# Optimization experiments

Hardware: AMD Instinct MI355X
Metric: run time of the kernel (lower is better)

## Reference

```python
import jax, jax.numpy as jnp
import numpy as np

# ---- static config ----
SCALES = [1, 2, 3, 4, 6, 9, 13, 19, 27, 40, 60, 88, 128]
L = sum(SCALES)            # 400
FIRST_L = SCALES[0]        # 1
C = 1024                   # emb_dim (C == D)
DEPTH = 8
H = 16
DH = C // H
CVAE = 64
V = 4096
ND = 256                   # node_embed_size
MLP = 4 * C
B = 32
EPS = 1e-6

_LVL = np.concatenate([np.full(pn, i, dtype=np.int32) for i, pn in enumerate(SCALES)])  # [L]
_BIAS = np.where(_LVL[:, None] >= _LVL[None, :], 0.0, -np.inf).astype(np.float32)        # [L,L]


def _ln(x):
    # LayerNorm without affine params (VAR's ln_wo_grad), eps=1e-6
    m = jnp.mean(x, axis=-1, keepdims=True)
    v = jnp.mean(jnp.square(x - m), axis=-1, keepdims=True)
    return (x - m) * jax.lax.rsqrt(v + EPS)


def setup_inputs() -> dict:
    key = jax.random.key(0)
    ks = iter(jax.random.split(key, 40))
    def p(shape, s=0.02):
        return jax.random.normal(next(ks), shape, dtype=jnp.float32) * s
    inp = {
        "x_BLCv_wo_first_l": jax.random.normal(next(ks), (B, L - FIRST_L, CVAE), jnp.float32),
        "poc_context": jax.random.normal(next(ks), (B, L, CVAE), jnp.float32),
        "poc_cond": jax.random.normal(next(ks), (B, ND), jnp.float32),
        # embedders / positional
        "word_w": p((CVAE, C)), "word_b": p((C,)),
        "poc_w": p((ND, C)), "poc_b": p((C,)),
        "pos_start": p((1, FIRST_L, C)),
        "pos_1LC": p((1, L, C)),
        "lvl_tab": p((len(SCALES), C)),
        # shared AdaLN (SiLU -> Linear(D, 6C))
        "ada_w": p((C, 6 * C)), "ada_b": p((6 * C,)),
        # per-block params, stacked over depth
        "ada_gss": p((DEPTH, 1, 1, 6, C)),
        "q_w": p((DEPTH, C, C)), "q_b": p((DEPTH, C)),
        "kv_w": p((DEPTH, C, 2 * C)), "kv_b": p((DEPTH, 2 * C)),
        "proj_w": p((DEPTH, C, C)), "proj_b": p((DEPTH, C)),
        "fc1_w": p((DEPTH, C, MLP)), "fc1_b": p((DEPTH, MLP)),
        "fc2_w": p((DEPTH, MLP, C)), "fc2_b": p((DEPTH, C)),
        # AdaLNBeforeHead (SiLU -> Linear(D, 2C)) + head
        "head_ada_w": p((C, 2 * C)), "head_ada_b": p((2 * C,)),
        "head_w": p((C, V)), "head_b": p((V,)),
    }
    return inp


def reference(x_BLCv_wo_first_l, poc_context, poc_cond,
              word_w, word_b, poc_w, poc_b, pos_start, pos_1LC, lvl_tab,
              ada_w, ada_b, ada_gss, q_w, q_b, kv_w, kv_b, proj_w, proj_b,
              fc1_w, fc1_b, fc2_w, fc2_b, head_ada_w, head_ada_b, head_w, head_b):
    lvl_idx = jnp.asarray(_LVL)
    bias = jnp.asarray(_BIAS)                      # [L,L] block scale-causal
    scale = 1.0 / np.sqrt(DH)

    cond = poc_cond @ poc_w + poc_b                # [B,C] (cond_BD == sos source)
    sos = cond[:, None, :] + pos_start             # [B,first_l,C]
    x = jnp.concatenate([sos, x_BLCv_wo_first_l @ word_w + word_b], axis=1)  # [B,L,C]
    lvl = lvl_tab[lvl_idx] + pos_1LC[0]            # [L,C]
    x = x + lvl
    poc = (poc_context @ word_w + word_b) + lvl    # [B,L,C]

    gss = jax.nn.silu(cond) @ ada_w + ada_b        # [B,6C]
    gss = gss.reshape(B, 1, 6, C)

    def block(x, params):
        ag, qw, qb, kvw, kvb, pw, pb, f1w, f1b, f2w, f2b = params
        mod = ag + gss                             # [B,1,6,C]
        g1, g2, s1, s2, sh1, sh2 = [mod[:, :, i] for i in range(6)]  # each [B,1,C]
        # cross-attention (q from modulated x, kv from poc context), scale-causal bias
        xn = _ln(x) * (1.0 + s1) + sh1
        q = (xn @ qw + qb).reshape(B, L, H, DH)
        kv = (poc @ kvw + kvb).reshape(B, L, 2, H, DH)
        k, v = kv[:, :, 0], kv[:, :, 1]
        att = jnp.einsum('bqhd,bkhd->bhqk', q, k) * scale + bias
        att = jax.nn.softmax(att, axis=-1)
        o = jnp.einsum('bhqk,bkhd->bqhd', att, v).reshape(B, L, C)
        x = x + g1 * (o @ pw + pb)
        # FFN with AdaLN modulation
        xn2 = _ln(x) * (1.0 + s2) + sh2
        hdn = jax.nn.gelu(xn2 @ f1w + f1b, approximate=False)
        x = x + g2 * (hdn @ f2w + f2b)
        return x, None

    x, _ = jax.lax.scan(block, x, (ada_gss, q_w, q_b, kv_w, kv_b, proj_w, proj_b,
                                   fc1_w, fc1_b, fc2_w, fc2_b))

    # AdaLNBeforeHead + head
    ss = jax.nn.silu(cond) @ head_ada_w + head_ada_b   # [B,2C]
    h_scale, h_shift = ss[:, None, :C], ss[:, None, C:]
    x = _ln(x) * (1.0 + h_scale) + h_shift
    logits = x @ head_w + head_b                       # [B,L,V]
    return logits
```

## Files before the change

### kernel.cpp

```cpp
#include <hip/hip_runtime.h>
#include <hip/hip_bf16.h>
#include <math.h>

#define DEV __device__ __forceinline__

typedef __attribute__((ext_vector_type(4))) float f32x4;
typedef __attribute__((ext_vector_type(8))) short bf16x8;
typedef __attribute__((ext_vector_type(4))) short s16x4;

static constexpr int Bz = 32, Lz = 400, Cz = 1024, MLPz = 4096;
static constexpr int BL = Bz * Lz;

DEV float bf2f(unsigned short u) {
  union { unsigned int i; float f; } v; v.i = ((unsigned int)u) << 16; return v.f;
}
DEV unsigned short f2bf(float f) {
  union { float f; unsigned int i; } v; v.f = f;
  unsigned int r = v.i + 0x7FFFu + ((v.i >> 16) & 1u);
  return (unsigned short)(r >> 16);
}

DEV int level_of(int l) {
  const int cum[13] = {1,3,6,10,16,25,38,57,84,124,184,272,400};
  int lv = 12;
  #pragma unroll
  for (int i = 12; i >= 0; i--) if (l < cum[i]) lv = i;
  return lv;
}
DEV int row_kmax(int l) {
  const int cum[13] = {1,3,6,10,16,25,38,57,84,124,184,272,400};
  int km = 400;
  #pragma unroll
  for (int i = 12; i >= 0; i--) if (l < cum[i]) km = cum[i];
  return km;
}

DEV void stage16(const unsigned short* g, unsigned short* l) {
#if __has_builtin(__builtin_amdgcn_global_load_lds)
  __builtin_amdgcn_global_load_lds((const __attribute__((address_space(1))) void*)g,
                                   (__attribute__((address_space(3))) void*)l, 16, 0, 0);
#else
  *(bf16x8*)l = *(const bf16x8*)g;
#endif
}

__global__ __launch_bounds__(256)
void tconv_k(const float* __restrict__ in, unsigned short* __restrict__ out, int K, int N)
{
  __shared__ float t[64][65];
  const int n0 = blockIdx.x * 64, k0 = blockIdx.y * 64;
  #pragma unroll
  for (int i = 0; i < 16; i++) {
    int idx = i * 256 + threadIdx.x;
    int r = idx >> 6, c = idx & 63;
    t[r][c] = in[(size_t)(k0 + r) * N + n0 + c];
  }
  __syncthreads();
  #pragma unroll
  for (int i = 0; i < 16; i++) {
    int idx = i * 256 + threadIdx.x;
    int rn = idx >> 6, ck = idx & 63;
    out[(size_t)(n0 + rn) * K + k0 + ck] = f2bf(t[ck][rn]);
  }
}

enum { EP_BF16 = 0, EP_GELU = 1, EP_RESID = 2, EP_F32 = 3, EP_KV = 4 };

template<int MODE>
__global__ __launch_bounds__(256, 2)
void gemm2_k(const unsigned short* __restrict__ A, const unsigned short* __restrict__ Bt,
             const float* __restrict__ bias, void* __restrict__ out,
             float* __restrict__ xres, const float* __restrict__ gsh,
             const float* __restrict__ gpb, unsigned short* __restrict__ vtb,
             int N, int K)
{
  __shared__ unsigned short As[128 * 64];
  __shared__ unsigned short Bs[128 * 64];
  const int tid = threadIdx.x;
  const int lane = tid & 63, wv = tid >> 6;
  const int row0 = blockIdx.x * 128, col0 = blockIdx.y * 128;
  const int wm = (wv >> 1) * 64, wn = (wv & 1) * 64;

  f32x4 acc[4][4] = {};

  for (int k0 = 0; k0 < K; k0 += 64) {
    #pragma unroll
    for (int i = 0; i < 4; i++) {
      int ch = i * 256 + tid;
      int r = ch >> 3;
      int c8 = (ch & 7) ^ (r & 7);
      stage16(A + (size_t)(row0 + r) * K + k0 + c8 * 8, As + ch * 8);
    }
    #pragma unroll
    for (int i = 0; i < 4; i++) {
      int ch = i * 256 + tid;
      int r = ch >> 3;
      int c8 = (ch & 7) ^ (r & 7);
      stage16(Bt + (size_t)(col0 + r) * K + k0 + c8 * 8, Bs + ch * 8);
    }
    __syncthreads();
    #pragma unroll
    for (int kk = 0; kk < 2; kk++) {
      bf16x8 af[4], bfr[4];
      const int bcol = kk * 64 + (lane >> 4) * 16;
      #pragma unroll
      for (int m = 0; m < 4; m++) {
        int r = wm + m * 16 + (lane & 15);
        af[m] = *(const bf16x8*)((char*)As + r * 128 + (bcol ^ ((r & 7) << 4)));
      }
      #pragma unroll
      for (int n = 0; n < 4; n++) {
        int r = wn + n * 16 + (lane & 15);
        bfr[n] = *(const bf16x8*)((char*)Bs + r * 128 + (bcol ^ ((r & 7) << 4)));
      }
      #pragma unroll
      for (int m = 0; m < 4; m++)
        #pragma unroll
        for (int n = 0; n < 4; n++)
          acc[m][n] = __builtin_amdgcn_mfma_f32_16x16x32_bf16(af[m], bfr[n], acc[m][n], 0, 0, 0);
    }
    __syncthreads();
  }

  const int rbase = row0 + wm + ((lane >> 4) << 2);
  const int cbase = col0 + wn + (lane & 15);
  #pragma unroll
  for (int n = 0; n < 4; n++) {
    int gcol = cbase + n * 16;
    float bv = bias[gcol];
    #pragma unroll
    for (int m = 0; m < 4; m++) {
      #pragma unroll
      for (int r = 0; r < 4; r++) {
        int grow = rbase + m * 16 + r;
        float v = acc[m][n][r] + bv;
        if constexpr (MODE == EP_BF16) {
          ((unsigned short*)out)[(size_t)grow * N + gcol] = f2bf(v);
        } else if constexpr (MODE == EP_GELU) {
          float g = 0.5f * v * (1.f + erff(v * 0.70710678118654752f));
          ((unsigned short*)out)[(size_t)grow * N + gcol] = f2bf(g);
        } else if constexpr (MODE == EP_RESID) {
          int b = grow / Lz;
          float g = gsh[gcol] + gpb[(size_t)b * 6144 + gcol];
          xres[(size_t)grow * Cz + gcol] += g * v;
        } else if constexpr (MODE == EP_KV) {
          if (gcol < 1024) {
            ((unsigned short*)out)[(size_t)grow * 1024 + gcol] = f2bf(v);
          } else {
            int b = grow / Lz, l = grow - b * Lz;
            int h = (gcol >> 6) & 15, d = gcol & 63;
            vtb[(((size_t)b * 16 + h) * 64 + d) * Lz + l] = f2bf(v);
          }
        } else {
          ((float*)out)[(size_t)grow * N + gcol] = v;
        }
      }
    }
  }
}

__global__ __launch_bounds__(256)
void ln_k(const float* __restrict__ x, unsigned short* __restrict__ out,
          const float* __restrict__ ssh, const float* __restrict__ spb, int sstride,
          const float* __restrict__ hsh, const float* __restrict__ hpb, int hstride)
{
  const int row = blockIdx.x, tid = threadIdx.x;
  const int b = row / Lz;
  const float* xr = x + (size_t)row * Cz;
  float v[4];
  float s = 0.f;
  #pragma unroll
  for (int i = 0; i < 4; i++) { v[i] = xr[tid + i * 256]; s += v[i]; }
  __shared__ float red[8];
  #pragma unroll
  for (int o = 32; o > 0; o >>= 1) s += __shfl_xor(s, o, 64);
  if ((tid & 63) == 0) red[tid >> 6] = s;
  __syncthreads();
  float mean = (red[0] + red[1] + red[2] + red[3]) * (1.f / 1024.f);
  float vs = 0.f;
  #pragma unroll
  for (int i = 0; i < 4; i++) { float d = v[i] - mean; vs += d * d; }
  #pragma unroll
  for (int o = 32; o > 0; o >>= 1) vs += __shfl_xor(vs, o, 64);
  __syncthreads();
  if ((tid & 63) == 0) red[4 + (tid >> 6)] = vs;
  __syncthreads();
  float var = (red[4] + red[5] + red[6] + red[7]) * (1.f / 1024.f);
  float rstd = rsqrtf(var + 1e-6f);
  #pragma unroll
  for (int i = 0; i < 4; i++) {
    int c = tid + i * 256;
    float sc = (ssh ? ssh[c] : 0.f) + spb[(size_t)b * sstride + c];
    float sh = (hsh ? hsh[c] : 0.f) + hpb[(size_t)b * hstride + c];
    out[(size_t)row * Cz + c] = f2bf((v[i] - mean) * rstd * (1.f + sc) + sh);
  }
}

__global__ __launch_bounds__(512)
void attn3_k(const unsigned short* __restrict__ qb,
             const unsigned short* __restrict__ kbuf,
             const unsigned short* __restrict__ vtb,
             unsigned short* __restrict__ ob)
{
  __shared__ unsigned short Ks[400 * 64];
  __shared__ unsigned short Vt[64 * 408];
  __shared__ unsigned short Pl[8][512];
  const int bh = blockIdx.x, b = bh >> 4, h = bh & 15;
  const int qc = blockIdx.y;
  const int tid = threadIdx.x;
  const int q0 = qc * 128;
  const int nch = (row_kmax(min(q0 + 127, Lz - 1)) + 15) >> 4;

  const size_t kbase = (size_t)b * Lz * 1024 + h * 64;
  for (int i = tid; i < nch * 128; i += 512) {
    int l = i >> 3, d8 = i & 7;
    bf16x8 kr = *(const bf16x8*)&kbuf[kbase + (size_t)l * 1024 + d8 * 8];
    *(bf16x8*)((char*)Ks + l * 128 + ((d8 * 16) ^ ((l & 7) << 4))) = kr;
  }
  const size_t vbase = ((size_t)b * 16 + h) * 64 * Lz;
  for (int i = tid; i < 64 * 50; i += 512) {
    int d = i / 50, c8 = i - d * 50;
    *(bf16x8*)((char*)Vt + d * 816 + c8 * 16) = *(const bf16x8*)&vtb[vbase + (size_t)d * Lz + c8 * 8];
  }
  __syncthreads();

  const int wv = tid >> 6, lane = tid & 63, g = lane >> 4, q = lane & 15;
  const int qw0 = q0 + wv * 16;
  if (qw0 >= Lz) return;
  const int qrow = qw0 + q;
  const int my_kmax = row_kmax(qrow);
  const int nsch = (row_kmax(qw0 + 15) + 31) >> 5;

  const unsigned short* qp = qb + (size_t)(b * Lz + qrow) * Cz + h * 64;
  bf16x8 qf0 = *(const bf16x8*)(qp + g * 8);
  bf16x8 qf1 = *(const bf16x8*)(qp + 32 + g * 8);
  unsigned short* myP = &Pl[wv][0];

  float m = -1e30f, lsum = 0.f;
  f32x4 acc[4] = {};

  for (int sc = 0; sc < nsch; ++sc) {
    f32x4 st0 = {0.f,0.f,0.f,0.f}, st1 = {0.f,0.f,0.f,0.f};
    {
      int kr = sc * 32 + q;
      const char* kb = (const char*)Ks + kr * 128;
      int sw = (kr & 7) << 4;
      bf16x8 k0 = *(const bf16x8*)(kb + ((g * 16) ^ sw));
      bf16x8 k1 = *(const bf16x8*)(kb + ((64 + g * 16) ^ sw));
      st0 = __builtin_amdgcn_mfma_f32_16x16x32_bf16(k0, qf0, st0, 0, 0, 0);
      st0 = __builtin_amdgcn_mfma_f32_16x16x32_bf16(k1, qf1, st0, 0, 0, 0);
    }
    {
      int kr = sc * 32 + 16 + q;
      const char* kb = (const char*)Ks + kr * 128;
      int sw = (kr & 7) << 4;
      bf16x8 k0 = *(const bf16x8*)(kb + ((g * 16) ^ sw));
      bf16x8 k1 = *(const bf16x8*)(kb + ((64 + g * 16) ^ sw));
      st1 = __builtin_amdgcn_mfma_f32_16x16x32_bf16(k0, qf0, st1, 0, 0, 0);
      st1 = __builtin_amdgcn_mfma_f32_16x16x32_bf16(k1, qf1, st1, 0, 0, 0);
    }

    float s8[8]; float cmax = -1e30f;
    #pragma unroll
    for (int r = 0; r < 4; r++) {
      int k0g = sc * 32 + 4 * g + r;
      int k1g = k0g + 16;
      s8[r]     = (k0g < my_kmax) ? st0[r] * 0.125f : -1e30f;
      s8[4 + r] = (k1g < my_kmax) ? st1[r] * 0.125f : -1e30f;
      cmax = fmaxf(cmax, fmaxf(s8[r], s8[4 + r]));
    }
    cmax = fmaxf(cmax, __shfl_xor(cmax, 16, 64));
    cmax = fmaxf(cmax, __shfl_xor(cmax, 32, 64));
    float mnew = fmaxf(m, cmax);
    float f = __expf(m - mnew);
    float p[8], ps = 0.f;
    #pragma unroll
    for (int r = 0; r < 8; r++) { p[r] = __expf(s8[r] - mnew); ps += p[r]; }
    ps += __shfl_xor(ps, 16, 64);
    ps += __shfl_xor(ps, 32, 64);
    lsum = lsum * f + ps;
    m = mnew;
    #pragma unroll
    for (int blk = 0; blk < 4; blk++)
      #pragma unroll
      for (int j = 0; j < 4; j++) acc[blk][j] *= f;

    #pragma unroll
    for (int cp = 0; cp < 2; cp++) {
      #pragma unroll
      for (int j = 0; j < 2; j++) {
        unsigned int lo = f2bf(p[4 * cp + 2 * j]);
        unsigned int hi = f2bf(p[4 * cp + 2 * j + 1]);
        int w = 8 * cp + 2 * g + j;
        *(unsigned int*)((char*)myP + q * 64 + 4 * (w ^ q)) = lo | (hi << 16);
      }
    }

    unsigned int pw[4];
    #pragma unroll
    for (int i = 0; i < 4; i++)
      pw[i] = *(const unsigned int*)((const char*)myP + q * 64 + 4 * ((4 * g + i) ^ q));
    bf16x8 pfrag;
    #pragma unroll
    for (int i = 0; i < 4; i++) {
      pfrag[2 * i]     = (short)(pw[i] & 0xFFFF);
      pfrag[2 * i + 1] = (short)(pw[i] >> 16);
    }

    #pragma unroll
    for (int blk = 0; blk < 4; blk++) {
      bf16x8 vf = *(const bf16x8*)((const char*)Vt + (16 * blk + q) * 816 + (sc * 32 + 8 * g) * 2);
      acc[blk] = __builtin_amdgcn_mfma_f32_16x16x32_bf16(vf, pfrag, acc[blk], 0, 0, 0);
    }
  }

  float inv = 1.f / lsum;
  unsigned short* op = ob + (size_t)(b * Lz + qrow) * Cz + h * 64;
  #pragma unroll
  for (int blk = 0; blk < 4; blk++)
    #pragma unroll
    for (int r = 0; r < 4; r++)
      op[16 * blk + 4 * g + r] = f2bf(acc[blk][r] * inv);
}

__global__ __launch_bounds__(256)
void cond_k(const float* __restrict__ pc, const float* __restrict__ pw,
            const float* __restrict__ pb, float* __restrict__ cond,
            float* __restrict__ silu)
{
  const int b = blockIdx.y;
  const int n = blockIdx.x * 256 + threadIdx.x;
  __shared__ float a[256];
  a[threadIdx.x] = pc[b * 256 + threadIdx.x];
  __syncthreads();
  float s = pb[n];
  for (int k = 0; k < 256; k++) s += a[k] * pw[(size_t)k * Cz + n];
  cond[(size_t)b * Cz + n] = s;
  silu[(size_t)b * Cz + n] = s / (1.f + __expf(-s));
}

__global__ __launch_bounds__(256)
void smallmm_k(const float* __restrict__ A, const float* __restrict__ W,
               const float* __restrict__ bias, float* __restrict__ out, int N)
{
  const int b = blockIdx.y;
  const int n = blockIdx.x * 256 + threadIdx.x;
  __shared__ float a[1024];
  for (int i = threadIdx.x; i < 1024; i += 256) a[i] = A[(size_t)b * 1024 + i];
  __syncthreads();
  float s = bias[n];
  for (int k = 0; k < 1024; k++) s += a[k] * W[(size_t)k * N + n];
  out[(size_t)b * N + n] = s;
}

template<int MODE>
__global__ __launch_bounds__(256)
void embed_k(const float* __restrict__ src, const float* __restrict__ ww,
             const float* __restrict__ wb, const float* __restrict__ cond,
             const float* __restrict__ pos_start, const float* __restrict__ pos1,
             const float* __restrict__ ltab, void* __restrict__ out)
{
  const int r0 = blockIdx.x * 4;
  const int tid = threadIdx.x;
  const int b = r0 / Lz;
  __shared__ float a[4][64];
  {
    int rr = tid >> 6, k = tid & 63;
    int l = (r0 + rr) % Lz;
    float val;
    if (MODE == 0) val = (l == 0) ? 0.f : src[((size_t)b * (Lz - 1) + (l - 1)) * 64 + k];
    else           val = src[((size_t)(r0 + rr)) * 64 + k];
    a[rr][k] = val;
  }
  __syncthreads();
  #pragma unroll
  for (int ci = 0; ci < 4; ci++) {
    int c = tid + ci * 256;
    float s[4];
    #pragma unroll
    for (int rr = 0; rr < 4; rr++) {
      int l = (r0 + rr) % Lz;
      s[rr] = wb[c] + ltab[(size_t)level_of(l) * Cz + c] + pos1[(size_t)l * Cz + c];
    }
    for (int k = 0; k < 64; k++) {
      float w = ww[(size_t)k * Cz + c];
      #pragma unroll
      for (int rr = 0; rr < 4; rr++) s[rr] += a[rr][k] * w;
    }
    #pragma unroll
    for (int rr = 0; rr < 4; rr++) {
      int l = (r0 + rr) % Lz;
      if (MODE == 0) {
        float val = s[rr];
        if (l == 0) val = cond[(size_t)b * Cz + c] + pos_start[c] + ltab[c] + pos1[c];
        ((float*)out)[((size_t)(r0 + rr)) * Cz + c] = val;
      } else {
        ((unsigned short*)out)[((size_t)(r0 + rr)) * Cz + c] = f2bf(s[rr]);
      }
    }
  }
}

extern "C" void kernel_launch(void* const* d_in, const int* in_sizes, int n_in,
                              void* d_out, int out_size, void* d_ws, size_t ws_size,
                              hipStream_t stream)
{
  (void)in_sizes; (void)n_in; (void)out_size; (void)ws_size;
  const float* x_blcv   = (const float*)d_in[0];
  const float* poc_ctx  = (const float*)d_in[1];
  const float* poc_cond = (const float*)d_in[2];
  const float* word_w   = (const float*)d_in[3];
  const float* word_b   = (const float*)d_in[4];
  const float* poc_w    = (const float*)d_in[5];
  const float* poc_b    = (const float*)d_in[6];
  const float* pos_start= (const float*)d_in[7];
  const float* pos_1lc  = (const float*)d_in[8];
  const float* lvl_tab  = (const float*)d_in[9];
  const float* ada_w    = (const float*)d_in[10];
  const float* ada_b    = (const float*)d_in[11];
  const float* ada_gss  = (const float*)d_in[12];
  const float* q_w      = (const float*)d_in[13];
  const float* q_b      = (const float*)d_in[14];
  const float* kv_w     = (const float*)d_in[15];
  const float* kv_b     = (const float*)d_in[16];
  const float* proj_w   = (const float*)d_in[17];
  const float* proj_b   = (const float*)d_in[18];
  const float* fc1_w    = (const float*)d_in[19];
  const float* fc1_b    = (const float*)d_in[20];
  const float* fc2_w    = (const float*)d_in[21];
  const float* fc2_b    = (const float*)d_in[22];
  const float* head_ada_w = (const float*)d_in[23];
  const float* head_ada_b = (const float*)d_in[24];
  const float* head_w   = (const float*)d_in[25];
  const float* head_b   = (const float*)d_in[26];

  char* p = (char*)d_ws;
  auto carve = [&](size_t bytes) { void* r = (void*)p; p += (bytes + 255) & ~(size_t)255; return r; };
  float* x            = (float*)carve((size_t)BL * Cz * 4);
  unsigned short* xn  = (unsigned short*)carve((size_t)BL * Cz * 2);
  unsigned short* poc = (unsigned short*)carve((size_t)BL * Cz * 2);
  unsigned short* qbf = (unsigned short*)carve((size_t)BL * Cz * 2);
  unsigned short* kbuf= (unsigned short*)carve((size_t)BL * Cz * 2);
  unsigned short* vtb = (unsigned short*)carve((size_t)BL * Cz * 2);
  unsigned short* ob  = (unsigned short*)carve((size_t)BL * Cz * 2);
  unsigned short* hdn = (unsigned short*)carve((size_t)BL * MLPz * 2);
  unsigned short* wt  = (unsigned short*)carve((size_t)12582912 * 2);
  float* cond  = (float*)carve(32 * 1024 * 4);
  float* siluc = (float*)carve(32 * 1024 * 4);
  float* gss   = (float*)carve(32 * 6144 * 4);
  float* ss    = (float*)carve(32 * 2048 * 4);

  unsigned short* qwt  = wt;
  unsigned short* kvwt = wt + 1048576;
  unsigned short* pjwt = wt + 3145728;
  unsigned short* f1wt = wt + 4194304;
  unsigned short* f2wt = wt + 8388608;

  cond_k<<<dim3(4, 32), 256, 0, stream>>>(poc_cond, poc_w, poc_b, cond, siluc);
  smallmm_k<<<dim3(24, 32), 256, 0, stream>>>(siluc, ada_w, ada_b, gss, 6144);
  smallmm_k<<<dim3(8, 32), 256, 0, stream>>>(siluc, head_ada_w, head_ada_b, ss, 2048);
  embed_k<0><<<3200, 256, 0, stream>>>(x_blcv, word_w, word_b, cond, pos_start, pos_1lc, lvl_tab, x);
  embed_k<1><<<3200, 256, 0, stream>>>(poc_ctx, word_w, word_b, cond, pos_start, pos_1lc, lvl_tab, poc);

  for (int d = 0; d < 8; d++) {
    const float* ag = ada_gss + (size_t)d * 6144;
    tconv_k<<<dim3(16, 16), 256, 0, stream>>>(q_w + (size_t)d * 1048576, qwt, 1024, 1024);
    tconv_k<<<dim3(32, 16), 256, 0, stream>>>(kv_w + (size_t)d * 2097152, kvwt, 1024, 2048);
    tconv_k<<<dim3(16, 16), 256, 0, stream>>>(proj_w + (size_t)d * 1048576, pjwt, 1024, 1024);
    tconv_k<<<dim3(64, 16), 256, 0, stream>>>(fc1_w + (size_t)d * 4194304, f1wt, 1024, 4096);
    tconv_k<<<dim3(16, 64), 256, 0, stream>>>(fc2_w + (size_t)d * 4194304, f2wt, 4096, 1024);

    ln_k<<<BL, 256, 0, stream>>>(x, xn, ag + 2 * 1024, gss + 2 * 1024, 6144,
                                 ag + 4 * 1024, gss + 4 * 1024, 6144);
    gemm2_k<EP_BF16><<<dim3(100, 8), 256, 0, stream>>>(
        xn, qwt, q_b + d * 1024, qbf, nullptr, nullptr, nullptr, nullptr, 1024, 1024);
    gemm2_k<EP_KV><<<dim3(100, 16), 256, 0, stream>>>(
        poc, kvwt, kv_b + d * 2048, kbuf, nullptr, nullptr, nullptr, vtb, 2048, 1024);
    attn3_k<<<dim3(512, 4), 512, 0, stream>>>(qbf, kbuf, vtb, ob);
    gemm2_k<EP_RESID><<<dim3(100, 8), 256, 0, stream>>>(
        ob, pjwt, proj_b + d * 1024, nullptr, x, ag + 0, gss + 0, nullptr, 1024, 1024);
    ln_k<<<BL, 256, 0, stream>>>(x, xn, ag + 3 * 1024, gss + 3 * 1024, 6144,
                                 ag + 5 * 1024, gss + 5 * 1024, 6144);
    gemm2_k<EP_GELU><<<dim3(100, 32), 256, 0, stream>>>(
        xn, f1wt, fc1_b + d * 4096, hdn, nullptr, nullptr, nullptr, nullptr, 4096, 1024);
    gemm2_k<EP_RESID><<<dim3(100, 8), 256, 0, stream>>>(
        hdn, f2wt, fc2_b + d * 1024, nullptr, x, ag + 1024, gss + 1024, nullptr, 1024, 4096);
  }
  ln_k<<<BL, 256, 0, stream>>>(x, xn, nullptr, ss, 2048, nullptr, ss + 1024, 2048);
  tconv_k<<<dim3(64, 16), 256, 0, stream>>>(head_w, wt, 1024, 4096);
  gemm2_k<EP_F32><<<dim3(100, 32), 256, 0, stream>>>(
      xn, wt, head_b, d_out, nullptr, nullptr, nullptr, nullptr, 4096, 1024);
}
```

Before: 6.115 ms.

## Batch weight transposes, swizzle GEMM block order, vectorize LayerNorm loads

Merges four per-layer weight-transpose launches into one 3D-grid kernel that picks its matrix from blockIdx.z and exits early for out-of-range blocks. Remaps GEMM workgroup IDs with an XCD-style swizzle so consecutive blocks share A/B tiles in cache. LayerNorm now reads each thread's four contiguous floats with a single vector load. The swizzle hardcodes 100 row tiles and assumes the block count divides by 8.

```diff
diff --git a/kernel.cpp b/kernel.cpp
--- a/kernel.cpp
+++ b/kernel.cpp
@@ -64,6 +64,36 @@
   }
 }
 
+__global__ __launch_bounds__(256)
+void tconv4_k(const float* __restrict__ qw, const float* __restrict__ kvw,
+              const float* __restrict__ pjw, const float* __restrict__ f1w,
+              unsigned short* __restrict__ qwt, unsigned short* __restrict__ kvwt,
+              unsigned short* __restrict__ pjwt, unsigned short* __restrict__ f1wt)
+{
+  const int z = blockIdx.z;
+  const float* in; unsigned short* out; int N;
+  if (z == 0)      { in = qw;  out = qwt;  N = 1024; }
+  else if (z == 1) { in = kvw; out = kvwt; N = 2048; }
+  else if (z == 2) { in = pjw; out = pjwt; N = 1024; }
+  else             { in = f1w; out = f1wt; N = 4096; }
+  if ((int)blockIdx.x >= (N >> 6)) return;
+  __shared__ float t[64][65];
+  const int n0 = blockIdx.x * 64, k0 = blockIdx.y * 64;
+  #pragma unroll
+  for (int i = 0; i < 16; i++) {
+    int idx = i * 256 + threadIdx.x;
+    int r = idx >> 6, c = idx & 63;
+    t[r][c] = in[(size_t)(k0 + r) * N + n0 + c];
+  }
+  __syncthreads();
+  #pragma unroll
+  for (int i = 0; i < 16; i++) {
+    int idx = i * 256 + threadIdx.x;
+    int rn = idx >> 6, ck = idx & 63;
+    out[(size_t)(n0 + rn) * 1024 + k0 + ck] = f2bf(t[ck][rn]);
+  }
+}
+
 enum { EP_BF16 = 0, EP_GELU = 1, EP_RESID = 2, EP_F32 = 3, EP_KV = 4 };
 
 template<int MODE>
@@ -78,7 +108,13 @@
   __shared__ unsigned short Bs[128 * 64];
   const int tid = threadIdx.x;
   const int lane = tid & 63, wv = tid >> 6;
-  const int row0 = blockIdx.x * 128, col0 = blockIdx.y * 128;
+
+  const int nwg = gridDim.x * gridDim.y;
+  const int cpx = nwg >> 3;
+  const int bid = blockIdx.y * gridDim.x + blockIdx.x;
+  const int swz = (bid & 7) * cpx + (bid >> 3);
+  const int row0 = (swz % 100) * 128, col0 = (swz / 100) * 128;
+
   const int wm = (wv >> 1) * 64, wn = (wv & 1) * 64;
 
   f32x4 acc[4][4] = {};
@@ -167,10 +203,8 @@
   const int row = blockIdx.x, tid = threadIdx.x;
   const int b = row / Lz;
   const float* xr = x + (size_t)row * Cz;
-  float v[4];
-  float s = 0.f;
-  #pragma unroll
-  for (int i = 0; i < 4; i++) { v[i] = xr[tid + i * 256]; s += v[i]; }
+  f32x4 v = *(const f32x4*)(xr + tid * 4);
+  float s = v[0] + v[1] + v[2] + v[3];
   __shared__ float red[8];
   #pragma unroll
   for (int o = 32; o > 0; o >>= 1) s += __shfl_xor(s, o, 64);
@@ -189,7 +223,7 @@
   float rstd = rsqrtf(var + 1e-6f);
   #pragma unroll
   for (int i = 0; i < 4; i++) {
-    int c = tid + i * 256;
+    int c = tid * 4 + i;
     float sc = (ssh ? ssh[c] : 0.f) + spb[(size_t)b * sstride + c];
     float sh = (hsh ? hsh[c] : 0.f) + hpb[(size_t)b * hstride + c];
     out[(size_t)row * Cz + c] = f2bf((v[i] - mean) * rstd * (1.f + sc) + sh);
@@ -464,10 +498,10 @@
 
   for (int d = 0; d < 8; d++) {
     const float* ag = ada_gss + (size_t)d * 6144;
-    tconv_k<<<dim3(16, 16), 256, 0, stream>>>(q_w + (size_t)d * 1048576, qwt, 1024, 1024);
-    tconv_k<<<dim3(32, 16), 256, 0, stream>>>(kv_w + (size_t)d * 2097152, kvwt, 1024, 2048);
-    tconv_k<<<dim3(16, 16), 256, 0, stream>>>(proj_w + (size_t)d * 1048576, pjwt, 1024, 1024);
-    tconv_k<<<dim3(64, 16), 256, 0, stream>>>(fc1_w + (size_t)d * 4194304, f1wt, 1024, 4096);
+    tconv4_k<<<dim3(64, 16, 4), 256, 0, stream>>>(
+        q_w + (size_t)d * 1048576, kv_w + (size_t)d * 2097152,
+        proj_w + (size_t)d * 1048576, fc1_w + (size_t)d * 4194304,
+        qwt, kvwt, pjwt, f1wt);
     tconv_k<<<dim3(16, 64), 256, 0, stream>>>(fc2_w + (size_t)d * 4194304, f2wt, 4096, 1024);
 
     ln_k<<<BL, 256, 0, stream>>>(x, xn, ag + 2 * 1024, gss + 2 * 1024, 6144,
```

Measured after the change: 6.781 ms. +10.9%, slower.
